# Kernel tuning notes

Hardware: AMD Instinct MI355X
Metric: run time of the kernel (lower is better)

Reference implementation:

```python
import jax, jax.numpy as jnp
import numpy as np

N, F, C, H, HX = 100000, 500, 40, 256, 64
E = 1_600_000


def setup_inputs() -> dict:
    key = jax.random.key(0)
    ks = jax.random.split(key, 12)
    s = lambda fan_in: 1.0 / np.sqrt(fan_in)
    return {
        "x": jax.random.normal(ks[0], (N, F), dtype=jnp.float32),
        "y": jax.random.randint(ks[1], (N,), 0, C),
        "train_mask": jax.random.randint(ks[2], (N,), 0, 2).astype(bool),
        "edge_index": jax.random.randint(ks[3], (2, E), 0, N),
        "edge_index_neg": jax.random.randint(ks[4], (2, E), 0, N),
        "fc1_w": jax.random.uniform(ks[5], (H, F), jnp.float32, -s(F), s(F)),
        "fc1_b": jnp.zeros((H,), jnp.float32),
        "fc2_w": jax.random.uniform(ks[6], (C, H), jnp.float32, -s(H), s(H)),
        "fc2_b": jnp.zeros((C,), jnp.float32),
        "xenc_w": jax.random.uniform(ks[7], (HX, F), jnp.float32, -s(F), s(F)),
        "xenc_b": jnp.zeros((HX,), jnp.float32),
        "pexy_w": jax.random.uniform(ks[8], (1, 2 * (HX + C)), jnp.float32, -s(2 * (HX + C)), s(2 * (HX + C))),
        "pexy_b": jnp.zeros((1,), jnp.float32),
    }


def reference(x, y, train_mask, edge_index, edge_index_neg,
              fc1_w, fc1_b, fc2_w, fc2_b, xenc_w, xenc_b, pexy_w, pexy_b):
    temperature = 1.0
    # MLP p(y|x), inference mode (dropout is identity)
    h = jax.nn.relu(x @ fc1_w.T + fc1_b)
    logits = (h @ fc2_w.T + fc2_b) / temperature
    y_log_prob = jax.nn.log_softmax(logits, axis=-1)            # [N, C]
    y_prob = jnp.exp(y_log_prob)
    one_hot = jax.nn.one_hot(y, y_prob.shape[1], dtype=y_prob.dtype)
    y_prob = jnp.where(train_mask[:, None], one_hot, y_prob)    # [N, C]

    # node encoder
    xe = jax.nn.relu(x @ xenc_w.T + xenc_b)                     # [N, HX]

    # The scorer Linear(2*(HX+C) -> 1) applied to cat([x_q, x_k, y_q, y_k])
    # decomposes into per-node query/key scalars (same math, no big concat):
    hx = xe.shape[1]
    w = pexy_w[0]
    w_xq, w_xk = w[:hx], w[hx:2 * hx]
    w_yq, w_yk = w[2 * hx:2 * hx + y_prob.shape[1]], w[2 * hx + y_prob.shape[1]:]
    s_q = xe @ w_xq + y_prob @ w_yq                             # [N]
    s_k = xe @ w_xk + y_prob @ w_yk                             # [N]

    def edge_scores(ei):
        return (s_q[ei[0]] + s_k[ei[1]] + pexy_b[0])[:, None]   # [E, 1]

    e_pred_pos = edge_scores(edge_index)
    e_pred_neg = edge_scores(edge_index_neg)
    return (e_pred_pos, e_pred_neg, y_log_prob)
```

## Files before the change

### kernel.cpp

```cpp
#include <hip/hip_runtime.h>
#include <stdint.h>

#define N_NODES 100000
#define F_DIM   500
#define C_DIM   40
#define H_DIM   256
#define HX_DIM  64
#define O_DIM   320
#define E_NUM   1600000

typedef unsigned short u16;
typedef unsigned int   u32;
typedef __attribute__((ext_vector_type(4))) u16    u16x4;
typedef __attribute__((ext_vector_type(8))) u16    u16x8;
typedef __attribute__((ext_vector_type(4))) float  f32x4;
typedef __attribute__((ext_vector_type(8))) short  bf16x8;

__device__ __forceinline__ float bf2f(u16 v) {
  u32 u = ((u32)v) << 16;
  return __builtin_bit_cast(float, u);
}
__device__ __forceinline__ u16 f2bf(float f) {
  u32 x = __builtin_bit_cast(u32, f);
  x += 0x7fffu + ((x >> 16) & 1u);
  return (u16)(x >> 16);
}

__global__ __launch_bounds__(256) void k_detect(const u32* __restrict__ tm, int* __restrict__ flag)
{
  __shared__ int s;
  if (threadIdx.x == 0) s = 0;
  __syncthreads();
  int local = 0;
  #pragma unroll
  for (int j = 0; j < 16; ++j) {
    if (tm[j * 256 + threadIdx.x] > 1u) local = 1;
  }
  if (local) s = 1;
  __syncthreads();
  if (threadIdx.x == 0) *flag = s;
}

__global__ __launch_bounds__(256) void k_cvtw(
    const float* __restrict__ fc1w, const float* __restrict__ xencw, u16* __restrict__ wws)
{
  const int g = blockIdx.x * 256 + threadIdx.x;
  const int c = g / 1280;
  const int rem = g - c * 1280;
  const int r = rem >> 2;
  const int k0 = c * 32 + (rem & 3) * 8;
  const float* src = (r < H_DIM) ? (fc1w + (long)r * F_DIM)
                                 : (xencw + (long)(r - H_DIM) * F_DIM);
  f32x4 v0 = {0.f, 0.f, 0.f, 0.f}, v1 = v0;
  if (k0 + 4 <= F_DIM) v0 = *(const f32x4*)(src + k0);
  if (k0 + 8 <= F_DIM) v1 = *(const f32x4*)(src + k0 + 4);
  u16x8 o;
  #pragma unroll
  for (int i = 0; i < 4; ++i) { o[i] = f2bf(v0[i]); o[4 + i] = f2bf(v1[i]); }
  *(u16x8*)(wws + (size_t)g * 8) = o;
}

#define G_BM 64
#define G_BK 32
#define BN   320
#define RH_LD 328

__global__ __launch_bounds__(512, 4) void k_fused(
    const float* __restrict__ x, const u16* __restrict__ wws,
    const float* __restrict__ fc1b, const float* __restrict__ xencb,
    const int* __restrict__ y, const void* __restrict__ tmask,
    const float* __restrict__ fc2w, const float* __restrict__ fc2b,
    const float* __restrict__ pw, const int* __restrict__ mask_flag,
    float* __restrict__ out_lp, float* __restrict__ sq_out, float* __restrict__ sk_out)
{
  __shared__ __align__(16) u16 smem[36736];
  u16* sOut = smem;
  u16* sBp  = smem + 20992;

  const int tid  = threadIdx.x;
  const int lane = tid & 63;
  const int wid  = tid >> 6;
  const int wr   = wid >> 2;
  const int wcol = wid & 3;
  const int l15 = lane & 15, lgrp = lane >> 4;
  const long rowbase = (long)blockIdx.x * G_BM;

  long r0 = rowbase + wr * 32 + l15;
  long r1 = r0 + 16;
  if (r0 > N_NODES - 1) r0 = N_NODES - 1;
  if (r1 > N_NODES - 1) r1 = N_NODES - 1;
  const float* ap0 = x + r0 * F_DIM;
  const float* ap1 = x + r1 * F_DIM;

  const u16* bbase = wws + (wcol * 80 + l15) * 32 + lgrp * 8;

  f32x4 acc[2][5];
  #pragma unroll
  for (int m = 0; m < 2; ++m)
    #pragma unroll
    for (int n = 0; n < 5; ++n)
      acc[m][n] = (f32x4){0.f, 0.f, 0.f, 0.f};

  f32x4 a0l, a0h, a1l, a1h;
  bf16x8 bP[5], bQ[5];

#define LA(kc)                                                                 \
  {                                                                            \
    const int k0 = (kc) * G_BK + lgrp * 8;                                     \
    const int ka = (k0     > 496) ? 496 : k0;                                  \
    const int kb = (k0 + 4 > 496) ? 496 : (k0 + 4);                            \
    a0l = *(const f32x4*)(ap0 + ka);  a0h = *(const f32x4*)(ap0 + kb);         \
    a1l = *(const f32x4*)(ap1 + ka);  a1h = *(const f32x4*)(ap1 + kb);         \
  }

#define LB(dst, kc)                                                            \
  {                                                                            \
    const u16* bp = bbase + (size_t)(kc) * (BN * G_BK);                        \
    _Pragma("unroll")                                                          \
    for (int n = 0; n < 5; ++n) dst[n] = *(const bf16x8*)(bp + n * 512);       \
  }

#define GS(kc, BU, BL)                                                         \
  {                                                                            \
    bf16x8 af0, af1;                                                           \
    _Pragma("unroll")                                                          \
    for (int i = 0; i < 4; ++i) {                                              \
      af0[i]     = (short)f2bf(a0l[i]);  af0[4 + i] = (short)f2bf(a0h[i]);     \
      af1[i]     = (short)f2bf(a1l[i]);  af1[4 + i] = (short)f2bf(a1h[i]);     \
    }                                                                          \
    if ((kc) < 15) { LA((kc) + 1); LB(BL, (kc) + 1); }                         \
    _Pragma("unroll")                                                          \
    for (int n = 0; n < 5; ++n) {                                              \
      acc[0][n] = __builtin_amdgcn_mfma_f32_16x16x32_bf16(af0, BU[n], acc[0][n], 0, 0, 0); \
      acc[1][n] = __builtin_amdgcn_mfma_f32_16x16x32_bf16(af1, BU[n], acc[1][n], 0, 0, 0); \
    }                                                                          \
  }

  LA(0); LB(bP, 0);
  GS(0,  bP, bQ)  GS(1,  bQ, bP)  GS(2,  bP, bQ)  GS(3,  bQ, bP)
  GS(4,  bP, bQ)  GS(5,  bQ, bP)  GS(6,  bP, bQ)  GS(7,  bQ, bP)
  GS(8,  bP, bQ)  GS(9,  bQ, bP)  GS(10, bP, bQ)  GS(11, bQ, bP)
  GS(12, bP, bQ)  GS(13, bQ, bP)  GS(14, bP, bQ)  GS(15, bQ, bP)

  #pragma unroll
  for (int n = 0; n < 5; ++n) {
    const int col = wcol * 80 + n * 16 + l15;
    const float bias = (col < H_DIM) ? fc1b[col] : xencb[col - H_DIM];
    #pragma unroll
    for (int m = 0; m < 2; ++m) {
      const int rr0 = wr * 32 + m * 16 + lgrp * 4;
      #pragma unroll
      for (int rg = 0; rg < 4; ++rg)
        sOut[(rr0 + rg) * RH_LD + col] = f2bf(fmaxf(acc[m][n][rg] + bias, 0.f));
    }
  }
  #pragma unroll
  for (int it = 0; it < 4; ++it) {
    const int g = it * 512 + tid;
    if (g < 1920) {
      const int r = g / 40, c = g - r * 40;
      const int k0 = c * 8;
      u16x8 v = {0, 0, 0, 0, 0, 0, 0, 0};
      const float* src = nullptr;
      if (r < C_DIM) { if (k0 < H_DIM) src = fc2w + r * H_DIM + k0; }
      else if (r == C_DIM)     { if (k0 >= H_DIM) src = pw + (k0 - H_DIM); }
      else if (r == C_DIM + 1) { if (k0 >= H_DIM) src = pw + HX_DIM + (k0 - H_DIM); }
      if (src) {
        const f32x4 v0 = *(const f32x4*)src;
        const f32x4 v1 = *(const f32x4*)(src + 4);
        #pragma unroll
        for (int i = 0; i < 4; ++i) { v[i] = f2bf(v0[i]); v[4 + i] = f2bf(v1[i]); }
      }
      *(u16x8*)&sBp[r * RH_LD + c * 8] = v;
    }
  }
  __syncthreads();

  if (wid < 4) {
    f32x4 racc[3];
    #pragma unroll
    for (int n = 0; n < 3; ++n) racc[n] = (f32x4){0.f, 0.f, 0.f, 0.f};
    const u16* pa = &sOut[(wid * 16 + l15) * RH_LD + lgrp * 8];
    const u16* pb = &sBp[l15 * RH_LD + lgrp * 8];
    #pragma unroll
    for (int kc = 0; kc < 10; ++kc) {
      const bf16x8 a = *(const bf16x8*)(pa + kc * 32);
      #pragma unroll
      for (int n = 0; n < 3; ++n) {
        const bf16x8 b = *(const bf16x8*)(pb + n * 16 * RH_LD + kc * 32);
        racc[n] = __builtin_amdgcn_mfma_f32_16x16x32_bf16(a, b, racc[n], 0, 0, 0);
      }
    }

    const int c0 = l15, c1 = 16 + l15, c2 = 32 + l15;
    const bool v2 = (l15 < 8);
    const float b0 = fc2b[c0], b1 = fc2b[c1], b2 = v2 ? fc2b[c2] : 0.f;
    const float wq0 = pw[2 * HX_DIM + c0], wq1 = pw[2 * HX_DIM + c1],
                wq2 = v2 ? pw[2 * HX_DIM + c2] : 0.f;
    const float wk0 = pw[2 * HX_DIM + C_DIM + c0], wk1 = pw[2 * HX_DIM + C_DIM + c1],
                wk2 = v2 ? pw[2 * HX_DIM + C_DIM + c2] : 0.f;
    const bool byte_mask = (*mask_flag != 0);

    #pragma unroll
    for (int rg = 0; rg < 4; ++rg) {
      const long row = rowbase + wid * 16 + lgrp * 4 + rg;
      const bool rv = (row < N_NODES);
      const long rowc = rv ? row : (N_NODES - 1);
      const float lg0 = racc[0][rg] + b0;
      const float lg1 = racc[1][rg] + b1;
      const float lg2 = racc[2][rg] + b2;
      const float sxq = __shfl(racc[2][rg], (lane & 48) | 8, 64);
      const float sxk = __shfl(racc[2][rg], (lane & 48) | 9, 64);

      float m = fmaxf(lg0, lg1);
      if (v2) m = fmaxf(m, lg2);
      #pragma unroll
      for (int off = 1; off < 16; off <<= 1) m = fmaxf(m, __shfl_xor(m, off, 64));
      const float e0 = __expf(lg0 - m), e1 = __expf(lg1 - m),
                  e2 = v2 ? __expf(lg2 - m) : 0.f;
      float s = e0 + e1 + e2;
      #pragma unroll
      for (int off = 1; off < 16; off <<= 1) s += __shfl_xor(s, off, 64);
      const float lse = m + __logf(s);
      const float inv = 1.f / s;

      const int yv = y[rowc];
      const bool tm = byte_mask ? (((const unsigned char*)tmask)[rowc] != 0)
                                : (((const int*)tmask)[rowc] != 0);
      const float p0 = tm ? (c0 == yv ? 1.f : 0.f) : e0 * inv;
      const float p1 = tm ? (c1 == yv ? 1.f : 0.f) : e1 * inv;
      const float p2 = tm ? (c2 == yv ? 1.f : 0.f) : e2 * inv;
      float sq = p0 * wq0 + p1 * wq1 + p2 * wq2;
      float sk = p0 * wk0 + p1 * wk1 + p2 * wk2;
      #pragma unroll
      for (int off = 1; off < 16; off <<= 1) {
        sq += __shfl_xor(sq, off, 64);
        sk += __shfl_xor(sk, off, 64);
      }

      if (rv) {
        float* lp = out_lp + row * C_DIM;
        lp[c0] = lg0 - lse;
        lp[c1] = lg1 - lse;
        if (v2) lp[c2] = lg2 - lse;
        if (l15 == 0) { sq_out[row] = sq + sxq; sk_out[row] = sk + sxk; }
      }
    }
  }
#undef LA
#undef LB
#undef GS
}

__global__ __launch_bounds__(256) void k_edges(
    const int* __restrict__ ei, const int* __restrict__ ein,
    const float* __restrict__ sq, const float* __restrict__ sk,
    const float* __restrict__ pb, float* __restrict__ out)
{
  const int e = blockIdx.x * 256 + threadIdx.x;
  if (e >= E_NUM) return;
  const float b = pb[0];
  const int a0 = ei[e],  a1 = ei[E_NUM + e];
  out[e] = sq[a0] + sk[a1] + b;
  const int c0 = ein[e], c1 = ein[E_NUM + e];
  out[E_NUM + e] = sq[c0] + sk[c1] + b;
}

extern "C" void kernel_launch(void* const* d_in, const int* in_sizes, int n_in,
                              void* d_out, int out_size, void* d_ws, size_t ws_size,
                              hipStream_t stream)
{
  const float* x     = (const float*)d_in[0];
  const int*   y     = (const int*)d_in[1];
  const void*  tm    = d_in[2];
  const int*   ei    = (const int*)d_in[3];
  const int*   ein   = (const int*)d_in[4];
  const float* fc1w  = (const float*)d_in[5];
  const float* fc1b  = (const float*)d_in[6];
  const float* fc2w  = (const float*)d_in[7];
  const float* fc2b  = (const float*)d_in[8];
  const float* xencw = (const float*)d_in[9];
  const float* xencb = (const float*)d_in[10];
  const float* pw    = (const float*)d_in[11];
  const float* pb    = (const float*)d_in[12];
  float* out = (float*)d_out;

  float* sq   = (float*)((char*)d_ws + (size_t)N_NODES * O_DIM * 2);
  float* sk   = sq + N_NODES;
  int*   flag = (int*)(sk + N_NODES);
  u16*   wws  = (u16*)((char*)d_ws + 64800064);

  k_detect<<<1, 256, 0, stream>>>((const u32*)tm, flag);
  k_cvtw  <<<80, 256, 0, stream>>>(fc1w, xencw, wws);
  const int nrb = (N_NODES + G_BM - 1) / G_BM;
  k_fused <<<nrb, 512, 0, stream>>>(x, wws, fc1b, xencb, y, tm, fc2w, fc2b, pw, flag,
                                    out + 2 * (size_t)E_NUM, sq, sk);
  k_edges <<<E_NUM / 256, 256, 0, stream>>>(ei, ein, sq, sk, pb, out);
}
```

Baseline: 163.7 us.

## Stage x tile in swizzled LDS, shrink block to 32 rows, prepack fc2 weights

The fused MLP kernel now handles 32 rows per 256-thread block instead of 64 rows per 512 threads. It first loads the whole 32x500 x tile with coalesced row-wise reads, converts it to bf16 and stores it in XOR-swizzled shared memory, and the MFMA loop then reads A fragments from LDS rather than doing strided per-lane global loads. The fc2/pexy weights are converted to bf16 once in a new small pre-kernel and read from global memory with double buffering, so each block no longer rebuilds them in LDS. Shared memory per block shrinks, but the bounds clamping for the last tile is removed, which relies on N being a multiple of 32.

```diff
diff --git a/kernel.cpp b/kernel.cpp
--- a/kernel.cpp
+++ b/kernel.cpp
@@ -60,39 +60,76 @@
   *(u16x8*)(wws + (size_t)g * 8) = o;
 }
 
-#define G_BM 64
-#define G_BK 32
+__global__ __launch_bounds__(256) void k_cvtw2(
+    const float* __restrict__ fc2w, const float* __restrict__ pw, u16* __restrict__ wwsB)
+{
+  const int g = blockIdx.x * 256 + threadIdx.x;
+  if (g >= 1920) return;
+  const int kc = g / 192;
+  const int rem = g - kc * 192;
+  const int r = rem >> 2;
+  const int k0 = kc * 32 + (rem & 3) * 8;
+  const float* src = nullptr;
+  if (r < C_DIM)           { if (k0 + 8 <= H_DIM) src = fc2w + r * H_DIM + k0; }
+  else if (r == C_DIM)     { if (k0 >= H_DIM) src = pw + (k0 - H_DIM); }
+  else if (r == C_DIM + 1) { if (k0 >= H_DIM) src = pw + HX_DIM + (k0 - H_DIM); }
+  u16x8 o = {0, 0, 0, 0, 0, 0, 0, 0};
+  if (src) {
+    const f32x4 v0 = *(const f32x4*)src;
+    const f32x4 v1 = *(const f32x4*)(src + 4);
+    #pragma unroll
+    for (int i = 0; i < 4; ++i) { o[i] = f2bf(v0[i]); o[4 + i] = f2bf(v1[i]); }
+  }
+  *(u16x8*)(wwsB + (size_t)g * 8) = o;
+}
+
 #define BN   320
 #define RH_LD 328
 
-__global__ __launch_bounds__(512, 4) void k_fused(
-    const float* __restrict__ x, const u16* __restrict__ wws,
+__global__ __launch_bounds__(256, 4) void k_fused(
+    const float* __restrict__ x, const u16* __restrict__ wws, const u16* __restrict__ wwsB,
     const float* __restrict__ fc1b, const float* __restrict__ xencb,
     const int* __restrict__ y, const void* __restrict__ tmask,
-    const float* __restrict__ fc2w, const float* __restrict__ fc2b,
-    const float* __restrict__ pw, const int* __restrict__ mask_flag,
+    const float* __restrict__ fc2b, const float* __restrict__ pw,
+    const int* __restrict__ mask_flag,
     float* __restrict__ out_lp, float* __restrict__ sq_out, float* __restrict__ sk_out)
 {
-  __shared__ __align__(16) u16 smem[36736];
+  __shared__ __align__(16) u16 smem[16384];
   u16* sOut = smem;
-  u16* sBp  = smem + 20992;
 
   const int tid  = threadIdx.x;
   const int lane = tid & 63;
-  const int wid  = tid >> 6;
-  const int wr   = wid >> 2;
-  const int wcol = wid & 3;
+  const int wcol = tid >> 6;
   const int l15 = lane & 15, lgrp = lane >> 4;
-  const long rowbase = (long)blockIdx.x * G_BM;
-
-  long r0 = rowbase + wr * 32 + l15;
-  long r1 = r0 + 16;
-  if (r0 > N_NODES - 1) r0 = N_NODES - 1;
-  if (r1 > N_NODES - 1) r1 = N_NODES - 1;
-  const float* ap0 = x + r0 * F_DIM;
-  const float* ap1 = x + r1 * F_DIM;
-
-  const u16* bbase = wws + (wcol * 80 + l15) * 32 + lgrp * 8;
+  const long rowbase = (long)blockIdx.x * 32;
+
+  {
+    f32x4 v0[4], v1[4];
+    #pragma unroll
+    for (int half = 0; half < 2; ++half) {
+      #pragma unroll
+      for (int i = 0; i < 4; ++i) {
+        const int g = tid + 256 * (half * 4 + i);
+        const int r = g >> 6, c = g & 63;
+        const int k0 = c * 8;
+        v0[i] = (f32x4){0.f, 0.f, 0.f, 0.f};
+        v1[i] = v0[i];
+        const float* p = x + (rowbase + r) * F_DIM + k0;
+        if (k0 + 4 <= F_DIM) v0[i] = *(const f32x4*)p;
+        if (k0 + 8 <= F_DIM) v1[i] = *(const f32x4*)(p + 4);
+      }
+      #pragma unroll
+      for (int i = 0; i < 4; ++i) {
+        const int g = tid + 256 * (half * 4 + i);
+        const int r = g >> 6, c = g & 63;
+        const int phys = c ^ (r & 7);
+        u16x8 o;
+        #pragma unroll
+        for (int j = 0; j < 4; ++j) { o[j] = f2bf(v0[i][j]); o[4 + j] = f2bf(v1[i][j]); }
+        *(u16x8*)(smem + r * 512 + phys * 8) = o;
+      }
+    }
+  }
 
   f32x4 acc[2][5];
   #pragma unroll
@@ -101,46 +138,47 @@
     for (int n = 0; n < 5; ++n)
       acc[m][n] = (f32x4){0.f, 0.f, 0.f, 0.f};
 
-  f32x4 a0l, a0h, a1l, a1h;
-  bf16x8 bP[5], bQ[5];
-
-#define LA(kc)                                                                 \
-  {                                                                            \
-    const int k0 = (kc) * G_BK + lgrp * 8;                                     \
-    const int ka = (k0     > 496) ? 496 : k0;                                  \
-    const int kb = (k0 + 4 > 496) ? 496 : (k0 + 4);                            \
-    a0l = *(const f32x4*)(ap0 + ka);  a0h = *(const f32x4*)(ap0 + kb);         \
-    a1l = *(const f32x4*)(ap1 + ka);  a1h = *(const f32x4*)(ap1 + kb);         \
-  }
+  const u16* bbase = wws + (wcol * 80 + l15) * 32 + lgrp * 8;
+  const int arow_off = l15 * 512;
 
 #define LB(dst, kc)                                                            \
   {                                                                            \
-    const u16* bp = bbase + (size_t)(kc) * (BN * G_BK);                        \
+    const u16* bp = bbase + (size_t)(kc) * (BN * 32);                          \
     _Pragma("unroll")                                                          \
     for (int n = 0; n < 5; ++n) dst[n] = *(const bf16x8*)(bp + n * 512);       \
   }
 
-#define GS(kc, BU, BL)                                                         \
+#define LDA(A0, A1, kc)                                                        \
   {                                                                            \
-    bf16x8 af0, af1;                                                           \
-    _Pragma("unroll")                                                          \
-    for (int i = 0; i < 4; ++i) {                                              \
-      af0[i]     = (short)f2bf(a0l[i]);  af0[4 + i] = (short)f2bf(a0h[i]);     \
-      af1[i]     = (short)f2bf(a1l[i]);  af1[4 + i] = (short)f2bf(a1h[i]);     \
-    }                                                                          \
-    if ((kc) < 15) { LA((kc) + 1); LB(BL, (kc) + 1); }                         \
+    const int phys = (((kc) * 4 + lgrp) ^ (l15 & 7)) * 8;                      \
+    A0 = *(const bf16x8*)(smem + arow_off + phys);                             \
+    A1 = *(const bf16x8*)(smem + arow_off + 16 * 512 + phys);                  \
+  }
+
+#define GS(kc, AC0, AC1, AN0, AN1, BU, BL)                                     \
+  {                                                                            \
+    if ((kc) < 15) { LDA(AN0, AN1, (kc) + 1); LB(BL, (kc) + 1); }              \
     _Pragma("unroll")                                                          \
     for (int n = 0; n < 5; ++n) {                                              \
-      acc[0][n] = __builtin_amdgcn_mfma_f32_16x16x32_bf16(af0, BU[n], acc[0][n], 0, 0, 0); \
-      acc[1][n] = __builtin_amdgcn_mfma_f32_16x16x32_bf16(af1, BU[n], acc[1][n], 0, 0, 0); \
+      acc[0][n] = __builtin_amdgcn_mfma_f32_16x16x32_bf16(AC0, BU[n], acc[0][n], 0, 0, 0); \
+      acc[1][n] = __builtin_amdgcn_mfma_f32_16x16x32_bf16(AC1, BU[n], acc[1][n], 0, 0, 0); \
     }                                                                          \
   }
 
-  LA(0); LB(bP, 0);
-  GS(0,  bP, bQ)  GS(1,  bQ, bP)  GS(2,  bP, bQ)  GS(3,  bQ, bP)
-  GS(4,  bP, bQ)  GS(5,  bQ, bP)  GS(6,  bP, bQ)  GS(7,  bQ, bP)
-  GS(8,  bP, bQ)  GS(9,  bQ, bP)  GS(10, bP, bQ)  GS(11, bQ, bP)
-  GS(12, bP, bQ)  GS(13, bQ, bP)  GS(14, bP, bQ)  GS(15, bQ, bP)
+  bf16x8 aX0, aX1, aY0, aY1, bP[5], bQ[5];
+  __syncthreads();
+  LDA(aX0, aX1, 0); LB(bP, 0);
+
+  GS(0,  aX0, aX1, aY0, aY1, bP, bQ)  GS(1,  aY0, aY1, aX0, aX1, bQ, bP)
+  GS(2,  aX0, aX1, aY0, aY1, bP, bQ)  GS(3,  aY0, aY1, aX0, aX1, bQ, bP)
+  GS(4,  aX0, aX1, aY0, aY1, bP, bQ)  GS(5,  aY0, aY1, aX0, aX1, bQ, bP)
+  GS(6,  aX0, aX1, aY0, aY1, bP, bQ)  GS(7,  aY0, aY1, aX0, aX1, bQ, bP)
+  GS(8,  aX0, aX1, aY0, aY1, bP, bQ)  GS(9,  aY0, aY1, aX0, aX1, bQ, bP)
+  GS(10, aX0, aX1, aY0, aY1, bP, bQ)  GS(11, aY0, aY1, aX0, aX1, bQ, bP)
+  GS(12, aX0, aX1, aY0, aY1, bP, bQ)  GS(13, aY0, aY1, aX0, aX1, bQ, bP)
+  GS(14, aX0, aX1, aY0, aY1, bP, bQ)  GS(15, aY0, aY1, aX0, aX1, bQ, bP)
+
+  __syncthreads();
 
   #pragma unroll
   for (int n = 0; n < 5; ++n) {
@@ -148,49 +186,42 @@
     const float bias = (col < H_DIM) ? fc1b[col] : xencb[col - H_DIM];
     #pragma unroll
     for (int m = 0; m < 2; ++m) {
-      const int rr0 = wr * 32 + m * 16 + lgrp * 4;
+      const int r0 = m * 16 + lgrp * 4;
       #pragma unroll
       for (int rg = 0; rg < 4; ++rg)
-        sOut[(rr0 + rg) * RH_LD + col] = f2bf(fmaxf(acc[m][n][rg] + bias, 0.f));
+        sOut[(r0 + rg) * RH_LD + col] = f2bf(fmaxf(acc[m][n][rg] + bias, 0.f));
     }
   }
-  #pragma unroll
-  for (int it = 0; it < 4; ++it) {
-    const int g = it * 512 + tid;
-    if (g < 1920) {
-      const int r = g / 40, c = g - r * 40;
-      const int k0 = c * 8;
-      u16x8 v = {0, 0, 0, 0, 0, 0, 0, 0};
-      const float* src = nullptr;
-      if (r < C_DIM) { if (k0 < H_DIM) src = fc2w + r * H_DIM + k0; }
-      else if (r == C_DIM)     { if (k0 >= H_DIM) src = pw + (k0 - H_DIM); }
-      else if (r == C_DIM + 1) { if (k0 >= H_DIM) src = pw + HX_DIM + (k0 - H_DIM); }
-      if (src) {
-        const f32x4 v0 = *(const f32x4*)src;
-        const f32x4 v1 = *(const f32x4*)(src + 4);
-        #pragma unroll
-        for (int i = 0; i < 4; ++i) { v[i] = f2bf(v0[i]); v[4 + i] = f2bf(v1[i]); }
-      }
-      *(u16x8*)&sBp[r * RH_LD + c * 8] = v;
+  __syncthreads();
+
+  if (tid < 128) {
+    const int wid = tid >> 6;
+    const u16* bBase = wwsB + l15 * 32 + lgrp * 8;
+    f32x4 racc[3];
+    #pragma unroll
+    for (int n = 0; n < 3; ++n) racc[n] = (f32x4){0.f, 0.f, 0.f, 0.f};
+    const u16* pa = sOut + (wid * 16 + l15) * RH_LD + lgrp * 8;
+
+    bf16x8 bc[3], bn[3];
+    #pragma unroll
+    for (int n = 0; n < 3; ++n) bc[n] = *(const bf16x8*)(bBase + n * 512);
+
+#define RH(kc, BC, BN_)                                                        \
+    {                                                                          \
+      if ((kc) < 9) {                                                          \
+        _Pragma("unroll")                                                      \
+        for (int n = 0; n < 3; ++n)                                            \
+          BN_[n] = *(const bf16x8*)(bBase + ((kc) + 1) * 1536 + n * 512);      \
+      }                                                                        \
+      const bf16x8 a = *(const bf16x8*)(pa + (kc) * 32);                       \
+      _Pragma("unroll")                                                        \
+      for (int n = 0; n < 3; ++n)                                              \
+        racc[n] = __builtin_amdgcn_mfma_f32_16x16x32_bf16(a, BC[n], racc[n], 0, 0, 0); \
     }
-  }
-  __syncthreads();
-
-  if (wid < 4) {
-    f32x4 racc[3];
-    #pragma unroll
-    for (int n = 0; n < 3; ++n) racc[n] = (f32x4){0.f, 0.f, 0.f, 0.f};
-    const u16* pa = &sOut[(wid * 16 + l15) * RH_LD + lgrp * 8];
-    const u16* pb = &sBp[l15 * RH_LD + lgrp * 8];
-    #pragma unroll
-    for (int kc = 0; kc < 10; ++kc) {
-      const bf16x8 a = *(const bf16x8*)(pa + kc * 32);
-      #pragma unroll
-      for (int n = 0; n < 3; ++n) {
-        const bf16x8 b = *(const bf16x8*)(pb + n * 16 * RH_LD + kc * 32);
-        racc[n] = __builtin_amdgcn_mfma_f32_16x16x32_bf16(a, b, racc[n], 0, 0, 0);
-      }
-    }
+
+    RH(0, bc, bn) RH(1, bn, bc) RH(2, bc, bn) RH(3, bn, bc) RH(4, bc, bn)
+    RH(5, bn, bc) RH(6, bc, bn) RH(7, bn, bc) RH(8, bc, bn) RH(9, bn, bc)
+#undef RH
 
     const int c0 = l15, c1 = 16 + l15, c2 = 32 + l15;
     const bool v2 = (l15 < 8);
@@ -204,8 +235,6 @@
     #pragma unroll
     for (int rg = 0; rg < 4; ++rg) {
       const long row = rowbase + wid * 16 + lgrp * 4 + rg;
-      const bool rv = (row < N_NODES);
-      const long rowc = rv ? row : (N_NODES - 1);
       const float lg0 = racc[0][rg] + b0;
       const float lg1 = racc[1][rg] + b1;
       const float lg2 = racc[2][rg] + b2;
@@ -224,9 +253,9 @@
       const float lse = m + __logf(s);
       const float inv = 1.f / s;
 
-      const int yv = y[rowc];
-      const bool tm = byte_mask ? (((const unsigned char*)tmask)[rowc] != 0)
-                                : (((const int*)tmask)[rowc] != 0);
+      const int yv = y[row];
+      const bool tm = byte_mask ? (((const unsigned char*)tmask)[row] != 0)
+                                : (((const int*)tmask)[row] != 0);
       const float p0 = tm ? (c0 == yv ? 1.f : 0.f) : e0 * inv;
       const float p1 = tm ? (c1 == yv ? 1.f : 0.f) : e1 * inv;
       const float p2 = tm ? (c2 == yv ? 1.f : 0.f) : e2 * inv;
@@ -238,17 +267,15 @@
         sk += __shfl_xor(sk, off, 64);
       }
 
-      if (rv) {
-        float* lp = out_lp + row * C_DIM;
-        lp[c0] = lg0 - lse;
-        lp[c1] = lg1 - lse;
-        if (v2) lp[c2] = lg2 - lse;
-        if (l15 == 0) { sq_out[row] = sq + sxq; sk_out[row] = sk + sxk; }
-      }
+      float* lp = out_lp + row * C_DIM;
+      lp[c0] = lg0 - lse;
+      lp[c1] = lg1 - lse;
+      if (v2) lp[c2] = lg2 - lse;
+      if (l15 == 0) { sq_out[row] = sq + sxq; sk_out[row] = sk + sxk; }
     }
   }
-#undef LA
 #undef LB
+#undef LDA
 #undef GS
 }
 
@@ -289,11 +316,13 @@
   float* sk   = sq + N_NODES;
   int*   flag = (int*)(sk + N_NODES);
   u16*   wws  = (u16*)((char*)d_ws + 64800064);
+  u16*   wwsB = (u16*)((char*)d_ws + 65127744);
 
   k_detect<<<1, 256, 0, stream>>>((const u32*)tm, flag);
   k_cvtw  <<<80, 256, 0, stream>>>(fc1w, xencw, wws);
-  const int nrb = (N_NODES + G_BM - 1) / G_BM;
-  k_fused <<<nrb, 512, 0, stream>>>(x, wws, fc1b, xencb, y, tm, fc2w, fc2b, pw, flag,
-                                    out + 2 * (size_t)E_NUM, sq, sk);
+  k_cvtw2 <<<8, 256, 0, stream>>>(fc2w, pw, wwsB);
+  k_fused <<<N_NODES / 32, 256, 0, stream>>>(x, wws, wwsB, fc1b, xencb, y, tm,
+                                             fc2b, pw, flag,
+                                             out + 2 * (size_t)E_NUM, sq, sk);
   k_edges <<<E_NUM / 256, 256, 0, stream>>>(ei, ein, sq, sk, pb, out);
 }
```

New measurement: 153.7 us. -6.1%, faster.
